# Optimization experiments

Hardware: AMD Instinct MI355X
Metric: run time of the kernel (lower is better)

The kernel has to match this reference:

```python
import jax, jax.numpy as jnp
import numpy as np

K = 10          # neighbors per span
KTOK = 3        # heads used per span
D = 2.0         # token adjacency threshold
GAMMA = 1.0
MAX_WIDTH = 16
CAP = 128       # cap_spans_per_token
B, L, KTOK_TOTAL = 8, 128, 4


def _enumerate_spans(L, max_width):
    ar = np.arange(L)
    l_g, r_g = np.meshgrid(ar, ar, indexing='ij')
    mask = (r_g >= l_g) & (r_g - l_g + 1 <= max_width)
    l_idx = l_g[mask]
    r_idx = r_g[mask]
    S = l_idx.size
    span2id = np.full((L, L), -1, dtype=np.int64)
    span2id[l_idx, r_idx] = np.arange(S)
    return span2id, l_idx, r_idx, S


def _geom_matrix(L, max_width, span2id, l_idx, r_idx):
    # 8-neighborhood (l+/-1, r+/-1) adjacency over span ids, boolean (S,S)
    S = l_idx.size
    off = np.array([[-1, -1], [-1, 0], [-1, 1], [0, -1], [0, 1], [1, -1], [1, 0], [1, 1]])
    nl = l_idx[:, None] + off[None, :, 0]
    nr = r_idx[:, None] + off[None, :, 1]
    valid = (nl >= 0) & (nr >= 0) & (nl <= nr) & (nr < L) & (nr - nl + 1 <= max_width)
    s2 = span2id[np.clip(nl, 0, L - 1), np.clip(nr, 0, L - 1)]
    rows = np.broadcast_to(np.arange(S)[:, None], s2.shape)
    m = valid & (s2 >= 0)
    Geom = np.zeros((S, S), dtype=bool)
    Geom[rows[m], s2[m]] = True
    np.fill_diagonal(Geom, False)
    return Geom


SPAN2ID, L_IDX, R_IDX, S = _enumerate_spans(L, MAX_WIDTH)
GEOM = jnp.asarray(_geom_matrix(L, MAX_WIDTH, SPAN2ID, L_IDX, R_IDX))


def setup_inputs() -> dict:
    key = jax.random.key(0)
    k1, k2, k3 = jax.random.split(key, 3)
    head_indices = jax.random.randint(k1, (B, L, L, KTOK_TOTAL), 0, L)
    head_weights = jax.random.uniform(k2, (B, L, L, KTOK_TOTAL), dtype=jnp.float32)
    dist = jax.random.uniform(k3, (B, L, L), dtype=jnp.float32) * 8.0
    return {"head_indices": head_indices, "head_weights": head_weights, "dist": dist}


def reference(head_indices, head_weights, dist):
    l_idx = jnp.asarray(L_IDX)
    r_idx = jnp.asarray(R_IDX)
    # gather per-span head indices/weights: (B, S, Ktok)
    idx_all = head_indices[:, l_idx, r_idx, :KTOK]
    w_all = head_weights[:, l_idx, r_idx, :KTOK]
    valid1 = idx_all >= 0
    idx_safe = jnp.clip(idx_all, 0, None)
    w_all = w_all * valid1.astype(w_all.dtype)

    # scatter-add token->span dense matrices: (B, S, L)
    b_ix = jnp.arange(B)[:, None, None]
    s_ix = jnp.arange(S)[None, :, None]
    P_w = jnp.zeros((B, S, L), w_all.dtype).at[b_ix, s_ix, idx_safe].add(w_all)
    P_bin = jnp.zeros((B, S, L), jnp.float32).at[b_ix, s_ix, idx_safe].add(valid1.astype(jnp.float32))

    # token adjacency with self loops
    A = jnp.maximum((dist <= D).astype(jnp.float32), jnp.eye(L, dtype=jnp.float32))
    U_mask = jnp.einsum('bsl,blm->bsm', P_bin, A) > 0.0  # (B, S, L) spans hitting token m

    # top-1 head token -> span one-hot, with per-token span cap
    top1 = jnp.clip(idx_all[:, :, 0], 0, L - 1)
    top1_valid = (idx_all[:, :, 0] >= 0).astype(jnp.float32)
    E = jax.nn.one_hot(top1, L, dtype=jnp.float32) * top1_valid[..., None]  # (B, S, L)
    E = jnp.swapaxes(E, 1, 2)  # (B, L, S)
    E = E * (jnp.cumsum(E, axis=2) <= float(CAP)).astype(jnp.float32)

    # candidate matrix M: (B, S, S)
    M = jnp.einsum('bsl,blt->bst', U_mask.astype(jnp.float32), E) > 0.0
    diag = jnp.arange(S)
    M = M.at[:, diag, diag].set(False)
    M = M | GEOM[None]

    # gate scores Gate = P_w @ exp(-gamma*dist) @ P_w^T
    G = jnp.exp(-GAMMA * dist)
    A_pw = jnp.einsum('bsl,blm->bsm', P_w, G)
    Gate = jnp.einsum('bsm,btm->bst', A_pw, P_w)

    Gate_masked = jnp.where(M, Gate, -jnp.inf)
    topk_vals, topk_idx = jax.lax.top_k(Gate_masked, K)  # (B, S, K)
    N_mask = jnp.isfinite(topk_vals)
    N_idx = topk_idx.astype(jnp.int32)

    # self-loop fill for invalid slots
    rows = jnp.broadcast_to(jnp.arange(S, dtype=N_idx.dtype)[None, :, None], (B, S, K))
    N_idx = jnp.where(N_mask, N_idx, rows)
    N_mask = jnp.ones_like(N_mask)
    return N_idx, N_mask
```

## Files before the change

kernel.cpp:

```cpp
#include <hip/hip_runtime.h>
#include <stdint.h>

#define NB 8
#define LL 128
#define NS 1928
#define NK 10
#define WPB 4
#define SPW 2
#define SLOTS 32

__device__ __forceinline__ int span_id(int l, int r) {
    int off = (l <= 112) ? (l << 4) : (NS - (((128 - l) * (129 - l)) >> 1));
    return off + (r - l);
}

__device__ __forceinline__ float npexp_f32(float x) {
    const float magic = 12582912.0f;
    const float log2e = 1.442695040888963f;
    const float c1 = -6.93145752e-1f;
    const float c2 = -1.42860677e-6f;
    float t = __fmul_rn(x, log2e);
    float q = __fsub_rn(__fadd_rn(t, magic), magic);
    float r = __fmaf_rn(q, c1, x);
    r = __fmaf_rn(q, c2, r);
    float num = __fmaf_rn(r, 5.082762527590693718096e-04f, 6.757896990527504603057e-03f);
    num = __fmaf_rn(num, r, 5.114512081637298353406e-02f);
    num = __fmaf_rn(num, r, 2.473615434895520810817e-01f);
    num = __fmaf_rn(num, r, 7.257664613233124478488e-01f);
    num = __fmaf_rn(num, r, 9.999999999980870924916e-01f);
    float den = __fmaf_rn(r, 2.159509375685829852307e-02f, -2.742335390411667452936e-01f);
    den = __fmaf_rn(den, r, 1.0f);
    float p = __fdiv_rn(num, den);
    int qi = (int)q;
    return __fmul_rn(p, __int_as_float((127 + qi) << 23));
}

__device__ __forceinline__ float keyval(unsigned long long k) {
    return __uint_as_float((unsigned)(k >> 32));
}

__device__ __forceinline__ void wfence() {
    __builtin_amdgcn_wave_barrier();
    __threadfence_block();
    __builtin_amdgcn_wave_barrier();
}

__device__ int wave_partition_fast(unsigned long long* a, int* posL, int* posR,
                                   int pl, int pr, int lane) {
    int pm = pl + ((pr - pl) >> 1);
    unsigned long long vl = a[pl], vm = a[pm], vr = a[pr], tt;
    if (keyval(vm) < keyval(vl)) { tt = vm; vm = vl; vl = tt; }
    if (keyval(vr) < keyval(vm)) { tt = vr; vr = vm; vm = tt; }
    if (keyval(vm) < keyval(vl)) { tt = vm; vm = vl; vl = tt; }
    float vp = keyval(vm);
    unsigned long long vq = a[pr - 1];
    if (lane == 0) { a[pl] = vl; a[pr] = vr; a[pm] = vq; a[pr - 1] = vm; }
    wfence();

    unsigned long long lmask = (1ull << lane) - 1ull;
    int baseL = 0, baseR = 0;
    for (int p0 = pl; p0 <= pr; p0 += 64) {
        int pos = p0 + lane;
        bool inr = (pos <= pr);
        float v = inr ? keyval(a[pos]) : 0.0f;
        bool ge = inr && (pos > pl) && (pos < pr) && (v >= vp);
        bool le = inr && (pos <= pr - 2) && (v <= vp);
        unsigned long long bge = __ballot(ge);
        unsigned long long ble = __ballot(le);
        if (ge) posL[baseL + __popcll(bge & lmask)] = pos;
        if (le) posR[baseR + __popcll(ble & lmask)] = pos;
        baseL += __popcll(bge);
        baseR += __popcll(ble);
    }
    wfence();
    int totGE = baseL, totLE = baseR;
    int maxk = (totGE < totLE) ? totGE : totLE;
    int K = 0;
    for (int base = 0;; base += 64) {
        int k = base + lane;
        bool active = (k < maxk);
        int Lk = active ? posL[k] : 0x7fffffff;
        int Rk = active ? posR[totLE - 1 - k] : -1;
        bool sw = active && (Lk < Rk);
        unsigned long long bm = __ballot(sw);
        int nsw = (~bm == 0ull) ? 64 : (__ffsll((long long)~bm) - 1);
        if (sw && (lane < nsw)) {
            unsigned long long tl = a[Lk], tr = a[Rk];
            a[Lk] = tr; a[Rk] = tl;
        }
        K += nsw;
        if (nsw < 64) break;
    }
    wfence();
    int pi = posL[K];
    if (K > 0) { int rp = posR[totLE - K]; if (rp < pi) pi = rp; }
    if (lane == 0) { tt = a[pi]; a[pi] = a[pr - 1]; a[pr - 1] = tt; }
    wfence();
    return pi;
}

__device__ __forceinline__ void lane_sift(unsigned long long* h, int start, int hm) {
    unsigned long long tmp = h[start];
    int i = start, j = start + start;
    while (j <= hm) {
        if (j < hm && keyval(h[j]) < keyval(h[j + 1])) ++j;
        if (keyval(tmp) < keyval(h[j])) { h[i] = h[j]; i = j; j += j; }
        else break;
    }
    h[i] = tmp;
}

__device__ void wave_heap_top(unsigned long long* a, int lo, int hi, int needlo, int lane) {
    unsigned long long* h = a + lo - 1;
    int hm = hi - lo + 1;
    int half = hm >> 1;
    int maxlvl = 0; { int v = half; while (v >>= 1) ++maxlvl; }
    for (int lvl = maxlvl; lvl >= 0; --lvl) {
        int n0 = 1 << lvl;
        int n1 = (n0 << 1) - 1; if (n1 > half) n1 = half;
        for (int nb = n0; nb <= n1; nb += 64) {
            int node = nb + lane;
            if (node <= n1) lane_sift(h, node, hm);
        }
        wfence();
    }
    int E = hi - needlo + 1;
    if (E > hm - 1) E = hm - 1;
    if (lane == 0) {
        int m = hm;
        for (int e = 0; e < E; ++e) {
            unsigned long long tmp = h[m]; h[m] = h[1]; --m;
            int i = 1, j = 2;
            while (j <= m) {
                if (j < m && keyval(h[j]) < keyval(h[j + 1])) ++j;
                if (keyval(tmp) < keyval(h[j])) { h[i] = h[j]; i = j; j += j; }
                else break;
            }
            h[i] = tmp;
        }
    }
    wfence();
}

__device__ void wave_insertion(unsigned long long* a, int lo, int hi, int lane) {
    int len = hi - lo + 1;
    unsigned long long v = (lane < len) ? a[lo + lane] : 0ull;
    float fv = keyval(v);
    int rank = 0;
    for (int j = 0; j < len; ++j) {
        unsigned long long vj = __shfl(v, j, 64);
        float fj = keyval(vj);
        if ((fj < fv) || (fj == fv && j < lane)) ++rank;
    }
    wfence();
    if (lane < len) a[lo + rank] = v;
    wfence();
}

__device__ void wave_np_sort_top(unsigned long long* a, int n, int lane, int* stk,
                                 int* posL, int* posR) {
    int depth = 0; { int v = n; while (v >>= 1) ++depth; }
    depth *= 2;
    const int TOPLO = n - NK;
    int sp = 0;
    int lo = 0, hi = n - 1;
    for (;;) {
        while (hi - lo > 15) {
            if (depth-- < 0) {
                if (hi >= TOPLO) wave_heap_top(a, lo, hi, (lo > TOPLO ? lo : TOPLO), lane);
                goto pop;
            }
            {
                int pi = wave_partition_fast(a, posL, posR, lo, hi, lane);
                if (pi - lo < hi - pi) {
                    if (lane == 0) { stk[sp * 2] = pi + 1; stk[sp * 2 + 1] = hi; }
                    ++sp; hi = pi - 1;
                } else {
                    if (lane == 0) { stk[sp * 2] = lo; stk[sp * 2 + 1] = pi - 1; }
                    ++sp; lo = pi + 1;
                }
                wfence();
            }
        }
        if (hi > lo && hi >= TOPLO) wave_insertion(a, lo, hi, lane);
pop:
        if (sp == 0) break;
        --sp;
        lo = stk[sp * 2]; hi = stk[sp * 2 + 1];
    }
}

__global__ __launch_bounds__(256)
void build_tables_kernel(const int* __restrict__ hi, const float* __restrict__ hw,
                         float4* __restrict__ g_pack, uint16_t* __restrict__ g_lrc,
                         unsigned char* __restrict__ top1) {
    int j = blockIdx.x * 256 + threadIdx.x;
    if (j >= NB * LL * 16) return;
    int b = j >> 11;
    int lw = j & 2047;
    int l = lw >> 4, w = lw & 15, r = l + w;
    if (r >= LL) return;
    int sid = span_id(l, r);
    const int* hb = hi + b * LL * LL * 4;
    const float* wb = hw + b * LL * LL * 4;
    int4 iv = *(const int4*)(hb + (l * LL + r) * 4);
    float4 wv = *(const float4*)(wb + (l * LL + r) * 4);
    int ia = iv.x, ib = iv.y, ic = iv.z;
    float wa = wv.x, wb2 = wv.y, wc = wv.z;
    int m0, m1 = 255, m2 = 255;
    float W0, W1 = 0.f, W2 = 0.f;
    if (ia == ib && ib == ic) {
        m0 = ia; W0 = __fadd_rn(__fadd_rn(wa, wb2), wc);
    } else if (ia == ib) {
        float W = __fadd_rn(wa, wb2);
        if (ia < ic) { m0 = ia; W0 = W; m1 = ic; W1 = wc; }
        else         { m0 = ic; W0 = wc; m1 = ia; W1 = W; }
    } else if (ia == ic) {
        float W = __fadd_rn(wa, wc);
        if (ia < ib) { m0 = ia; W0 = W; m1 = ib; W1 = wb2; }
        else         { m0 = ib; W0 = wb2; m1 = ia; W1 = W; }
    } else if (ib == ic) {
        float W = __fadd_rn(wb2, wc);
        if (ia < ib) { m0 = ia; W0 = wa; m1 = ib; W1 = W; }
        else         { m0 = ib; W0 = W; m1 = ia; W1 = wa; }
    } else {
        int x0 = ia, x1 = ib, x2 = ic; float y0 = wa, y1 = wb2, y2 = wc;
        if (x0 > x1) { int tx = x0; x0 = x1; x1 = tx; float ty = y0; y0 = y1; y1 = ty; }
        if (x1 > x2) { int tx = x1; x1 = x2; x2 = tx; float ty = y1; y1 = y2; y2 = ty; }
        if (x0 > x1) { int tx = x0; x0 = x1; x1 = tx; float ty = y0; y0 = y1; y1 = ty; }
        m0 = x0; m1 = x1; m2 = x2; W0 = y0; W1 = y1; W2 = y2;
    }
    uint32_t rec = (uint32_t)m0 | ((uint32_t)m1 << 8) | ((uint32_t)m2 << 16)
                 | ((uint32_t)(ia & 127) << 24);
    g_pack[b * NS + sid] = make_float4(W0, W1, W2, __uint_as_float(rec));
    g_lrc[b * NS + sid] = (uint16_t)(l | (r << 7));
    top1[b * NS + sid] = (unsigned char)(ia & 127);
}

__global__ void cap_kernel(const unsigned char* __restrict__ top1,
                           unsigned char* __restrict__ flags) {
    int gw = (blockIdx.x * blockDim.x + threadIdx.x) >> 6;
    int lane = threadIdx.x & 63;
    int b = gw >> 7, l = gw & 127;
    const unsigned char* tb = top1 + b * NS;
    unsigned char* fb = flags + b * NS;
    int cnt = 0;
    for (int t0 = 0; t0 < NS; t0 += 64) {
        int t = t0 + lane;
        int tp = (t < NS) ? (int)tb[t] : 255;
        bool match = (tp == l);
        unsigned long long m = __ballot(match);
        if (match) {
            int pre = __popcll(m & ((1ull << lane) - 1ull));
            fb[t] = (cnt + pre + 1 <= 128) ? 1 : 0;
        }
        cnt += __popcll(m);
    }
}

__device__ __forceinline__ void load_tables(const float4* __restrict__ gp,
                                            const uint16_t* __restrict__ gl,
                                            const unsigned char* __restrict__ fb,
                                            float4* s_pack, uint16_t* s_lrc) {
    for (int j = threadIdx.x; j < NS; j += 256) {
        float4 v = gp[j];
        uint32_t rec = __float_as_uint(v.w) | ((uint32_t)(fb[j] & 1) << 31);
        v.w = __uint_as_float(rec);
        s_pack[j] = v;
        s_lrc[j] = gl[j];
    }
}

__device__ __forceinline__ void span_prologue(const float* __restrict__ db, float4 ps,
                                              int lane, float* qrow, int stride,
                                              unsigned long long* ub) {
    uint32_t rec = __float_as_uint(ps.w);
    int m0 = rec & 255, m1 = (rec >> 8) & 255, m2 = (rec >> 16) & 255;
    bool e1 = (m1 != 255), e2 = (m2 != 255);
    const float* row0 = db + m0 * LL;
    const float* row1 = db + (e1 ? m1 : 0) * LL;
    const float* row2 = db + (e2 ? m2 : 0) * LL;
    int mA = lane, mB = lane + 64;
    float dA0 = row0[mA], dB0 = row0[mB];
    float dA1 = row1[mA], dB1 = row1[mB];
    float dA2 = row2[mA], dB2 = row2[mB];
    float qA = __fmaf_rn(ps.x, npexp_f32(-dA0), 0.0f);
    qA = __fmaf_rn(ps.y, npexp_f32(-dA1), qA);
    qA = __fmaf_rn(ps.z, npexp_f32(-dA2), qA);
    float qB = __fmaf_rn(ps.x, npexp_f32(-dB0), 0.0f);
    qB = __fmaf_rn(ps.y, npexp_f32(-dB1), qB);
    qB = __fmaf_rn(ps.z, npexp_f32(-dB2), qB);
    bool cA = (dA0 <= 2.0f || mA == m0) ||
              (e1 && (dA1 <= 2.0f || mA == m1)) ||
              (e2 && (dA2 <= 2.0f || mA == m2));
    bool cB = (dB0 <= 2.0f || mB == m0) ||
              (e1 && (dB1 <= 2.0f || mB == m1)) ||
              (e2 && (dB2 <= 2.0f || mB == m2));
    ub[0] = __ballot(cA);
    ub[1] = __ballot(cB);
    qrow[mA * stride] = qA;
    qrow[mB * stride] = qB;
}

__device__ __forceinline__ void topk_merge(unsigned key, int t0, int lane,
                                           unsigned& v, int& vi, unsigned& tau) {
    unsigned long long bm = __ballot(key > tau);
    while (bm) {
        int ln = __ffsll((long long)bm) - 1;
        bm &= bm - 1;
        unsigned kk = (unsigned)__builtin_amdgcn_readlane((int)key, ln);
        if (kk > tau) {
            int tk = t0 + ln;
            unsigned vprev = (unsigned)__builtin_amdgcn_update_dpp(
                -1, (int)v, 0x138 , 0xF, 0xF, false);
            int iprev = __builtin_amdgcn_update_dpp(
                0, vi, 0x138 , 0xF, 0xF, false);
            bool keep = (v >= kk);
            bool fp = (vprev < kk);
            v = keep ? v : (fp ? vprev : kk);
            vi = keep ? vi : (fp ? iprev : tk);
            tau = (unsigned)__builtin_amdgcn_readlane((int)v, 10);
        }
    }
}

__device__ __forceinline__ void span_epilogue(unsigned v, int vi, int b, int s, int lane,
                                              unsigned char* __restrict__ rowflag,
                                              int* __restrict__ out) {
    unsigned vn = __shfl_down(v, 1, 64);
    bool tie = (lane < NK) && (v != 0u) && (vn == v);
    bool flag = (__ballot(tie) != 0ull);
    if (lane < NK) {
        int o = (b * NS + s) * NK + lane;
        out[NB * NS * NK + o] = 1;
        if (!flag) out[o] = (vi >= 0) ? vi : s;
    }
    if (lane == 0) rowflag[b * NS + s] = flag ? 1 : 0;
}

__global__ __launch_bounds__(256)
void span_scan_kernel(const float4* __restrict__ g_pack,
                      const uint16_t* __restrict__ g_lrc,
                      const float* __restrict__ dist,
                      const unsigned char* __restrict__ capf,
                      unsigned char* __restrict__ rowflag,
                      int* __restrict__ out) {
    __shared__ float4 s_pack[NS];
    __shared__ uint16_t s_lrc[NS];
    __shared__ float2 s_q2[WPB][LL];

    const int b = blockIdx.y;
    load_tables(g_pack + b * NS, g_lrc + b * NS, capf + b * NS, s_pack, s_lrc);
    __syncthreads();

    const int wid = threadIdx.x >> 6;
    const int lane = threadIdx.x & 63;
    const int base = blockIdx.x * (WPB * SPW);
    const int sA = base + wid;
    const int sB = base + WPB + wid;
    const int sAchunk = sA & ~63;
    const int sBchunk = sB & ~63;

    const float* db = dist + b * LL * LL;
    unsigned long long ubA0, ubA1, ubB0, ubB1;
    {
        unsigned long long ub[2];
        span_prologue(db, s_pack[sA], lane, &s_q2[wid][0].x, 2, ub);
        ubA0 = ub[0]; ubA1 = ub[1];
        span_prologue(db, s_pack[sB], lane, &s_q2[wid][0].y, 2, ub);
        ubB0 = ub[0]; ubB1 = ub[1];
    }
    uint32_t lrcA = s_lrc[sA], lrcB = s_lrc[sB];
    int lsA = lrcA & 127, rsA = (lrcA >> 7) & 127;
    int lsB = lrcB & 127, rsB = (lrcB >> 7) & 127;
    const float2* qq = s_q2[wid];

    unsigned vA = 0u, vB = 0u; int viA = -1, viB = -1; unsigned tauA = 0u, tauB = 0u;

    for (int t0 = 0; t0 < NS; t0 += 64) {
        int t = t0 + lane;
        unsigned keyA = 0u, keyB = 0u;
        if (t < NS) {
            float4 pt = s_pack[t];
            uint32_t rt = __float_as_uint(pt.w);
            int i0 = rt & 127, i1 = (rt >> 8) & 127, i2 = (rt >> 16) & 127;
            float2 q0 = qq[i0], q1 = qq[i1], q2 = qq[i2];
            uint32_t lr = s_lrc[t];
            int lt = lr & 127, rt2 = (lr >> 7) & 127;
            int rb = (int)(rt >> 24);
            bool cum = ((int)rt) < 0;
            {
                float g = __fmaf_rn(pt.x, q0.x, 0.0f);
                g = __fmaf_rn(pt.y, q1.x, g);
                g = __fmaf_rn(pt.z, q2.x, g);
                int dl = lt - lsA; if (dl < 0) dl = -dl;
                int dr = rt2 - rsA; if (dr < 0) dr = -dr;
                bool geom = (dl <= 1) && (dr <= 1);
                unsigned long long bits = (rb & 64) ? ubA1 : ubA0;
                bool um = (((bits >> (rb & 63)) & 1ull) != 0) && cum;
                if (um || geom) keyA = __float_as_uint(g);
            }
            {
                float g = __fmaf_rn(pt.x, q0.y, 0.0f);
                g = __fmaf_rn(pt.y, q1.y, g);
                g = __fmaf_rn(pt.z, q2.y, g);
                int dl = lt - lsB; if (dl < 0) dl = -dl;
                int dr = rt2 - rsB; if (dr < 0) dr = -dr;
                bool geom = (dl <= 1) && (dr <= 1);
                unsigned long long bits = (rb & 64) ? ubB1 : ubB0;
                bool um = (((bits >> (rb & 63)) & 1ull) != 0) && cum;
                if (um || geom) keyB = __float_as_uint(g);
            }
            if (t0 == sAchunk) keyA = (t == sA) ? 0u : keyA;
            if (t0 == sBchunk) keyB = (t == sB) ? 0u : keyB;
        }
        topk_merge(keyA, t0, lane, vA, viA, tauA);
        topk_merge(keyB, t0, lane, vB, viB, tauB);
    }

    span_epilogue(vA, viA, b, sA, lane, rowflag, out);
    span_epilogue(vB, viB, b, sB, lane, rowflag, out);
}

__global__ __launch_bounds__(256)
void span_slow_kernel(const float4* __restrict__ g_pack,
                      const uint16_t* __restrict__ g_lrc,
                      const float* __restrict__ dist,
                      const unsigned char* __restrict__ capf,
                      const unsigned char* __restrict__ rowflag,
                      int* __restrict__ out) {
    __shared__ int s_nrows;
    __shared__ int s_rows[64];
    __shared__ float4 s_pack[NS];
    __shared__ uint16_t s_lrc[NS];
    __shared__ float s_qq[LL];
    __shared__ unsigned long long s_cov[2];
    __shared__ unsigned long long s_buf[NS];
    __shared__ int s_posL[NS], s_posR[NS];
    __shared__ int s_stk[48];

    const int b = blockIdx.x;
    const int slot = blockIdx.y;
    const unsigned char* rf = rowflag + b * NS;

    if (threadIdx.x < 64) {
        int lane = threadIdx.x;
        int i = slot + lane * SLOTS;
        bool f = (i < NS) && (rf[i] != 0);
        unsigned long long m = __ballot(f);
        if (f) s_rows[__popcll(m & ((1ull << lane) - 1ull))] = i;
        if (lane == 0) s_nrows = __popcll(m);
    }
    __syncthreads();
    int nrows = s_nrows;
    if (nrows == 0) return;

    load_tables(g_pack + b * NS, g_lrc + b * NS, capf + b * NS, s_pack, s_lrc);
    __syncthreads();

    const int wid = threadIdx.x >> 6;
    const int lane = threadIdx.x & 63;
    const float* db = dist + b * LL * LL;

    for (int ri = 0; ri < nrows; ++ri) {
        const int s = s_rows[ri];
        uint32_t lrc = s_lrc[s];
        int ls = lrc & 127, rs = (lrc >> 7) & 127;

        if (wid == 0) {
            unsigned long long ub[2];
            span_prologue(db, s_pack[s], lane, s_qq, 1, ub);
            if (lane == 0) { s_cov[0] = ub[0]; s_cov[1] = ub[1]; }
        }
        __syncthreads();
        unsigned long long ub0 = s_cov[0], ub1 = s_cov[1];

        for (int t = threadIdx.x; t < NS; t += 256) {
            float4 pt = s_pack[t];
            uint32_t rt = __float_as_uint(pt.w);
            float g = __fmaf_rn(pt.x, s_qq[rt & 127], 0.0f);
            g = __fmaf_rn(pt.y, s_qq[(rt >> 8) & 127], g);
            g = __fmaf_rn(pt.z, s_qq[(rt >> 16) & 127], g);
            uint32_t lr = s_lrc[t];
            int lt = lr & 127, rt2 = (lr >> 7) & 127;
            int dl = lt - ls; if (dl < 0) dl = -dl;
            int dr = rt2 - rs; if (dr < 0) dr = -dr;
            bool neq = (t != s);
            bool geom = neq && (dl <= 1) && (dr <= 1);
            int rb = (int)(rt >> 24);
            unsigned long long bits = (rb & 64) ? ub1 : ub0;
            bool um = (((bits >> (rb & 63)) & 1ull) != 0) && (((int)rt) < 0) && neq;
            unsigned h32 = (um || geom) ? __float_as_uint(g) : 0xFF800000u;
            s_buf[t] = ((unsigned long long)h32 << 32) | (unsigned)t;
        }
        __syncthreads();

        if (wid == 0) {
            wave_np_sort_top(s_buf, NS, lane, s_stk, s_posL, s_posR);
            if (lane < NK) {
                unsigned long long k = s_buf[NS - 1 - lane];
                int idx = ((unsigned)(k >> 32) == 0xFF800000u) ? s : (int)(k & 0xffffffffull);
                out[(b * NS + s) * NK + lane] = idx;
            }
        }
        __syncthreads();
    }
}

extern "C" void kernel_launch(void* const* d_in, const int* in_sizes, int n_in,
                              void* d_out, int out_size, void* d_ws, size_t ws_size,
                              hipStream_t stream) {
    const int* hi = (const int*)d_in[0];
    const float* hw = (const float*)d_in[1];
    const float* dist = (const float*)d_in[2];
    int* out = (int*)d_out;

    unsigned char* ws = (unsigned char*)d_ws;
    unsigned char* top1 = ws;
    unsigned char* capf = ws + NB * NS;
    unsigned char* rowflag = ws + 2 * NB * NS;
    float4* g_pack = (float4*)(ws + 3 * NB * NS);
    uint16_t* g_lrc = (uint16_t*)(ws + 3 * NB * NS + NB * NS * 16);

    build_tables_kernel<<<(NB * LL * 16) / 256, 256, 0, stream>>>(hi, hw, g_pack, g_lrc, top1);
    cap_kernel<<<(NB * LL * 64) / 256, 256, 0, stream>>>(top1, capf);
    dim3 grid(NS / (WPB * SPW), NB);
    span_scan_kernel<<<grid, 256, 0, stream>>>(g_pack, g_lrc, dist, capf, rowflag, out);
    dim3 sgrid(NB, SLOTS);
    span_slow_kernel<<<sgrid, 256, 0, stream>>>(g_pack, g_lrc, dist, capf, rowflag, out);
}
```

Before: 199.4 us.

## Process four spans per wave and move geometric neighbors to a post-scan merge

Each wave now handles four query spans instead of two, sharing the per-candidate float4 loads and q-table gathers across four gate computations packed in a float4 table. The geometric 8-neighborhood test is removed from the inner loop; after the scan, the up-to-8 geometric neighbors are evaluated explicitly and merged into the top-k with a new index-carrying merge, skipping those already counted via the union mask. The lrc table is no longer staged in shared memory, and the grid is rounded up with bounds guards. This cuts per-candidate ALU and LDS work and block count, at the cost of more registers per thread, which may reduce occupancy, plus serialized top-k merges across four spans.

```diff
diff --git a/kernel.cpp b/kernel.cpp
--- a/kernel.cpp
+++ b/kernel.cpp
@@ -6,7 +6,7 @@
 #define NS 1928
 #define NK 10
 #define WPB 4
-#define SPW 2
+#define SPW 4
 #define SLOTS 32
 
 __device__ __forceinline__ int span_id(int l, int r) {
@@ -37,6 +37,10 @@
 
 __device__ __forceinline__ float keyval(unsigned long long k) {
     return __uint_as_float((unsigned)(k >> 32));
+}
+
+__device__ __forceinline__ float f4c(const float4& v, int x) {
+    return x == 0 ? v.x : (x == 1 ? v.y : (x == 2 ? v.z : v.w));
 }
 
 __device__ __forceinline__ void wfence() {
@@ -324,6 +328,28 @@
     }
 }
 
+__device__ __forceinline__ void topk_merge_idx(unsigned key, int tval,
+                                               unsigned& v, int& vi, unsigned& tau) {
+    unsigned long long bm = __ballot(key > tau);
+    while (bm) {
+        int ln = __ffsll((long long)bm) - 1;
+        bm &= bm - 1;
+        unsigned kk = (unsigned)__builtin_amdgcn_readlane((int)key, ln);
+        if (kk > tau) {
+            int tk = __builtin_amdgcn_readlane(tval, ln);
+            unsigned vprev = (unsigned)__builtin_amdgcn_update_dpp(
+                -1, (int)v, 0x138, 0xF, 0xF, false);
+            int iprev = __builtin_amdgcn_update_dpp(
+                0, vi, 0x138, 0xF, 0xF, false);
+            bool keep = (v >= kk);
+            bool fp = (vprev < kk);
+            v = keep ? v : (fp ? vprev : kk);
+            vi = keep ? vi : (fp ? iprev : tk);
+            tau = (unsigned)__builtin_amdgcn_readlane((int)v, 10);
+        }
+    }
+}
+
 __device__ __forceinline__ void span_epilogue(unsigned v, int vi, int b, int s, int lane,
                                               unsigned char* __restrict__ rowflag,
                                               int* __restrict__ out) {
@@ -346,80 +372,105 @@
                       unsigned char* __restrict__ rowflag,
                       int* __restrict__ out) {
     __shared__ float4 s_pack[NS];
-    __shared__ uint16_t s_lrc[NS];
-    __shared__ float2 s_q2[WPB][LL];
+    __shared__ float4 s_q4[WPB][LL];
 
     const int b = blockIdx.y;
-    load_tables(g_pack + b * NS, g_lrc + b * NS, capf + b * NS, s_pack, s_lrc);
+    {
+        const float4* gp = g_pack + b * NS;
+        const unsigned char* fb = capf + b * NS;
+        for (int j = threadIdx.x; j < NS; j += 256) {
+            float4 v = gp[j];
+            v.w = __uint_as_float(__float_as_uint(v.w) | ((uint32_t)(fb[j] & 1) << 31));
+            s_pack[j] = v;
+        }
+    }
     __syncthreads();
 
     const int wid = threadIdx.x >> 6;
     const int lane = threadIdx.x & 63;
     const int base = blockIdx.x * (WPB * SPW);
-    const int sA = base + wid;
-    const int sB = base + WPB + wid;
-    const int sAchunk = sA & ~63;
-    const int sBchunk = sB & ~63;
-
     const float* db = dist + b * LL * LL;
-    unsigned long long ubA0, ubA1, ubB0, ubB1;
-    {
+    const uint16_t* glb = g_lrc + b * NS;
+
+    int ss[SPW]; bool ok[SPW]; int schunk[SPW];
+    int lsv[SPW], rsv[SPW];
+    unsigned long long ub0[SPW], ub1[SPW];
+
+    #pragma unroll
+    for (int x = 0; x < SPW; ++x) {
+        int s = base + x * WPB + wid;
+        ok[x] = (s < NS);
+        s = ok[x] ? s : 0;
+        ss[x] = s;
+        schunk[x] = s & ~63;
+        uint32_t lrc = glb[s];
+        lsv[x] = lrc & 127;
+        rsv[x] = (lrc >> 7) & 127;
         unsigned long long ub[2];
-        span_prologue(db, s_pack[sA], lane, &s_q2[wid][0].x, 2, ub);
-        ubA0 = ub[0]; ubA1 = ub[1];
-        span_prologue(db, s_pack[sB], lane, &s_q2[wid][0].y, 2, ub);
-        ubB0 = ub[0]; ubB1 = ub[1];
-    }
-    uint32_t lrcA = s_lrc[sA], lrcB = s_lrc[sB];
-    int lsA = lrcA & 127, rsA = (lrcA >> 7) & 127;
-    int lsB = lrcB & 127, rsB = (lrcB >> 7) & 127;
-    const float2* qq = s_q2[wid];
-
-    unsigned vA = 0u, vB = 0u; int viA = -1, viB = -1; unsigned tauA = 0u, tauB = 0u;
+        span_prologue(db, s_pack[s], lane, (float*)&s_q4[wid][0] + x, 4, ub);
+        ub0[x] = ub[0]; ub1[x] = ub[1];
+    }
+    const float4* qq = s_q4[wid];
+
+    unsigned v[SPW] = {0u, 0u, 0u, 0u};
+    int vi[SPW] = {-1, -1, -1, -1};
+    unsigned tau[SPW] = {0u, 0u, 0u, 0u};
 
     for (int t0 = 0; t0 < NS; t0 += 64) {
         int t = t0 + lane;
-        unsigned keyA = 0u, keyB = 0u;
+        unsigned key[SPW] = {0u, 0u, 0u, 0u};
         if (t < NS) {
             float4 pt = s_pack[t];
             uint32_t rt = __float_as_uint(pt.w);
-            int i0 = rt & 127, i1 = (rt >> 8) & 127, i2 = (rt >> 16) & 127;
-            float2 q0 = qq[i0], q1 = qq[i1], q2 = qq[i2];
-            uint32_t lr = s_lrc[t];
-            int lt = lr & 127, rt2 = (lr >> 7) & 127;
+            float4 q0 = qq[rt & 127];
+            float4 q1 = qq[(rt >> 8) & 127];
+            float4 q2 = qq[(rt >> 16) & 127];
+            int sh = (int)((rt >> 24) & 63);
+            bool hi2 = ((rt >> 24) & 64) != 0;
+            bool cum = ((int)rt) < 0;
+            #pragma unroll
+            for (int x = 0; x < SPW; ++x) {
+                float g = __fmaf_rn(pt.x, f4c(q0, x), 0.0f);
+                g = __fmaf_rn(pt.y, f4c(q1, x), g);
+                g = __fmaf_rn(pt.z, f4c(q2, x), g);
+                unsigned long long bits = hi2 ? ub1[x] : ub0[x];
+                bool um = (((bits >> sh) & 1ull) != 0) && cum;
+                key[x] = um ? __float_as_uint(g) : 0u;
+            }
+            #pragma unroll
+            for (int x = 0; x < SPW; ++x)
+                if (t0 == schunk[x]) key[x] = (t == ss[x]) ? 0u : key[x];
+        }
+        #pragma unroll
+        for (int x = 0; x < SPW; ++x)
+            topk_merge(key[x], t0, lane, v[x], vi[x], tau[x]);
+    }
+
+    {
+        int j = lane + (lane >= 4 ? 1 : 0);
+        int dl = j / 3 - 1, dr = j % 3 - 1;
+        #pragma unroll
+        for (int x = 0; x < SPW; ++x) {
+            int nl = lsv[x] + dl, nr = rsv[x] + dr;
+            bool valid = (lane < 8) && (nl >= 0) && (nr >= nl) && (nr < LL)
+                         && (nr - nl < 16);
+            int tg = valid ? span_id(nl, nr) : 0;
+            float4 pt = s_pack[tg];
+            uint32_t rt = __float_as_uint(pt.w);
+            float g = __fmaf_rn(pt.x, f4c(qq[rt & 127], x), 0.0f);
+            g = __fmaf_rn(pt.y, f4c(qq[(rt >> 8) & 127], x), g);
+            g = __fmaf_rn(pt.z, f4c(qq[(rt >> 16) & 127], x), g);
             int rb = (int)(rt >> 24);
-            bool cum = ((int)rt) < 0;
-            {
-                float g = __fmaf_rn(pt.x, q0.x, 0.0f);
-                g = __fmaf_rn(pt.y, q1.x, g);
-                g = __fmaf_rn(pt.z, q2.x, g);
-                int dl = lt - lsA; if (dl < 0) dl = -dl;
-                int dr = rt2 - rsA; if (dr < 0) dr = -dr;
-                bool geom = (dl <= 1) && (dr <= 1);
-                unsigned long long bits = (rb & 64) ? ubA1 : ubA0;
-                bool um = (((bits >> (rb & 63)) & 1ull) != 0) && cum;
-                if (um || geom) keyA = __float_as_uint(g);
-            }
-            {
-                float g = __fmaf_rn(pt.x, q0.y, 0.0f);
-                g = __fmaf_rn(pt.y, q1.y, g);
-                g = __fmaf_rn(pt.z, q2.y, g);
-                int dl = lt - lsB; if (dl < 0) dl = -dl;
-                int dr = rt2 - rsB; if (dr < 0) dr = -dr;
-                bool geom = (dl <= 1) && (dr <= 1);
-                unsigned long long bits = (rb & 64) ? ubB1 : ubB0;
-                bool um = (((bits >> (rb & 63)) & 1ull) != 0) && cum;
-                if (um || geom) keyB = __float_as_uint(g);
-            }
-            if (t0 == sAchunk) keyA = (t == sA) ? 0u : keyA;
-            if (t0 == sBchunk) keyB = (t == sB) ? 0u : keyB;
-        }
-        topk_merge(keyA, t0, lane, vA, viA, tauA);
-        topk_merge(keyB, t0, lane, vB, viB, tauB);
-    }
-
-    span_epilogue(vA, viA, b, sA, lane, rowflag, out);
-    span_epilogue(vB, viB, b, sB, lane, rowflag, out);
+            unsigned long long bits = (rb & 64) ? ub1[x] : ub0[x];
+            bool um = (((bits >> (rb & 63)) & 1ull) != 0) && (((int)rt) < 0);
+            unsigned key = (valid && !um) ? __float_as_uint(g) : 0u;
+            topk_merge_idx(key, tg, v[x], vi[x], tau[x]);
+        }
+    }
+
+    #pragma unroll
+    for (int x = 0; x < SPW; ++x)
+        if (ok[x]) span_epilogue(v[x], vi[x], b, ss[x], lane, rowflag, out);
 }
 
 __global__ __launch_bounds__(256)
@@ -524,7 +575,7 @@
 
     build_tables_kernel<<<(NB * LL * 16) / 256, 256, 0, stream>>>(hi, hw, g_pack, g_lrc, top1);
     cap_kernel<<<(NB * LL * 64) / 256, 256, 0, stream>>>(top1, capf);
-    dim3 grid(NS / (WPB * SPW), NB);
+    dim3 grid((NS + WPB * SPW - 1) / (WPB * SPW), NB);
     span_scan_kernel<<<grid, 256, 0, stream>>>(g_pack, g_lrc, dist, capf, rowflag, out);
     dim3 sgrid(NB, SLOTS);
     span_slow_kernel<<<sgrid, 256, 0, stream>>>(g_pack, g_lrc, dist, capf, rowflag, out);
```

Result: faster. 193.0 us (-3.2%).
